# Kernel optimization log

Hardware: AMD Instinct MI355X
Metric: run time of the kernel (lower is better)

Reference implementation:

```python
import jax, jax.numpy as jnp
jax.config.update("jax_enable_x64", True)  # original computes in float64
import numpy as np

ALPHA = 0.01  # init kwarg


def setup_inputs() -> dict:
    key = jax.random.key(0)
    x = jax.random.normal(key, (8, 8192, 512), dtype=jnp.float32)
    return {"x": x}


def reference(x):
    # x: [B, T, C]
    _, t, _ = x.shape
    # powers = flip(arange(t)) = [t-1, t-2, ..., 0]
    powers = jnp.arange(t - 1, -1, -1, dtype=jnp.float64)
    base = jnp.power(1.0 - ALPHA, powers)          # (1-alpha)^(t-1-i), [T]
    divisor = base.reshape(1, t, 1)                # [1, T, 1]
    weights = base.at[1:].multiply(ALPHA).reshape(1, t, 1)
    out = jnp.cumsum(x.astype(jnp.float64) * weights, axis=1) / divisor
    return out.astype(x.dtype)
```

## Files before the change

kernel.cpp:

```cpp
#include <hip/hip_runtime.h>
#include <math.h>


namespace {
constexpr int B = 8;
constexpr int T = 8192;
constexpr int C = 512;
constexpr float ALPHA = 0.01f;
constexpr float DECAY = 1.0f - ALPHA;
constexpr int CHUNK = 32;
constexpr int K = T / CHUNK;
constexpr int STRIDE4 = C / 4;
constexpr int TPB = C / 4;
constexpr int CTILE = 16;
}

__global__ __launch_bounds__(TPB) void ema_ends_kernel(const float* __restrict__ x,
                                                       float* __restrict__ ends) {
    const int k = blockIdx.x;
    const int b = blockIdx.y;
    const int tid = threadIdx.x;
    const float4* xp = reinterpret_cast<const float4*>(x) +
                       (size_t)(b * T + k * CHUNK) * STRIDE4 + tid;
    float4 y;
    if (k == 0) {
        y = xp[0];
    } else {
        y = make_float4(0.f, 0.f, 0.f, 0.f);
    }
#pragma unroll 8
    for (int t = 0; t < CHUNK; ++t) {
        float4 v = xp[(size_t)t * STRIDE4];
        y.x = DECAY * y.x + ALPHA * v.x;
        y.y = DECAY * y.y + ALPHA * v.y;
        y.z = DECAY * y.z + ALPHA * v.z;
        y.w = DECAY * y.w + ALPHA * v.w;
    }
    reinterpret_cast<float4*>(ends)[(size_t)(b * K + k) * STRIDE4 + tid] = y;
}

__global__ __launch_bounds__(TPB) void ema_carry_kernel(float* __restrict__ ends,
                                                        float decay_chunk) {
    const int b = blockIdx.x;
    const int tid = threadIdx.x;
    float4* ep = reinterpret_cast<float4*>(ends) + (size_t)b * K * STRIDE4 + tid;
    float4 y = make_float4(0.f, 0.f, 0.f, 0.f);
    static_assert(K % CTILE == 0, "");
    for (int base = 0; base < K; base += CTILE) {
        float4 e[CTILE];
#pragma unroll
        for (int i = 0; i < CTILE; ++i)
            e[i] = ep[(size_t)(base + i) * STRIDE4];
#pragma unroll
        for (int i = 0; i < CTILE; ++i) {
            y.x = decay_chunk * y.x + e[i].x;
            y.y = decay_chunk * y.y + e[i].y;
            y.z = decay_chunk * y.z + e[i].z;
            y.w = decay_chunk * y.w + e[i].w;
            ep[(size_t)(base + i) * STRIDE4] = y;
        }
    }
}

__global__ __launch_bounds__(TPB) void ema_scan_kernel(const float* __restrict__ x,
                                                       const float* __restrict__ ends,
                                                       float* __restrict__ out) {
    const int k = blockIdx.x;
    const int b = blockIdx.y;
    const int tid = threadIdx.x;
    const size_t base4 = (size_t)(b * T + k * CHUNK) * STRIDE4 + tid;
    const float4* xp = reinterpret_cast<const float4*>(x) + base4;
    float4* op = reinterpret_cast<float4*>(out) + base4;

    float4 y;
    if (k == 0) {
        y = xp[0];
    } else {
        y = reinterpret_cast<const float4*>(ends)[(size_t)(b * K + (k - 1)) * STRIDE4 + tid];
    }
#pragma unroll 8
    for (int t = 0; t < CHUNK; ++t) {
        float4 v = xp[(size_t)t * STRIDE4];
        y.x = DECAY * y.x + ALPHA * v.x;
        y.y = DECAY * y.y + ALPHA * v.y;
        y.z = DECAY * y.z + ALPHA * v.z;
        y.w = DECAY * y.w + ALPHA * v.w;
        op[(size_t)t * STRIDE4] = y;
    }
}

__global__ __launch_bounds__(TPB) void ema_seq_kernel(const float* __restrict__ x,
                                                      float* __restrict__ out) {
    const int b = blockIdx.x;
    const int tid = threadIdx.x;
    const float4* xp = reinterpret_cast<const float4*>(x) + (size_t)b * T * STRIDE4 + tid;
    float4* op = reinterpret_cast<float4*>(out) + (size_t)b * T * STRIDE4 + tid;
    float4 y = xp[0];
    for (int t = 0; t < T; ++t) {
        float4 v = xp[(size_t)t * STRIDE4];
        y.x = DECAY * y.x + ALPHA * v.x;
        y.y = DECAY * y.y + ALPHA * v.y;
        y.z = DECAY * y.z + ALPHA * v.z;
        y.w = DECAY * y.w + ALPHA * v.w;
        op[(size_t)t * STRIDE4] = y;
    }
}

extern "C" void kernel_launch(void* const* d_in, const int* in_sizes, int n_in,
                              void* d_out, int out_size, void* d_ws, size_t ws_size,
                              hipStream_t stream) {
    (void)in_sizes; (void)n_in; (void)out_size;
    const float* x = reinterpret_cast<const float*>(d_in[0]);
    float* out = reinterpret_cast<float*>(d_out);

    const size_t ws_need = (size_t)B * K * C * sizeof(float);
    const float decay_chunk = (float)pow((double)DECAY, (double)CHUNK);

    if (ws_size >= ws_need) {
        float* ends = reinterpret_cast<float*>(d_ws);
        ema_ends_kernel<<<dim3(K, B), dim3(TPB), 0, stream>>>(x, ends);
        ema_carry_kernel<<<dim3(B), dim3(TPB), 0, stream>>>(ends, decay_chunk);
        ema_scan_kernel<<<dim3(K, B), dim3(TPB), 0, stream>>>(x, ends, out);
    } else {
        ema_seq_kernel<<<dim3(B), dim3(TPB), 0, stream>>>(x, out);
    }
}
```

Baseline: 268.9 us.

## Fuse EMA scan into single-pass decoupled look-back kernel

```diff
diff --git a/kernel.cpp b/kernel.cpp
--- a/kernel.cpp
+++ b/kernel.cpp
@@ -12,51 +12,144 @@
 constexpr int K = T / CHUNK;
 constexpr int STRIDE4 = C / 4;
 constexpr int TPB = C / 4;
-constexpr int CTILE = 16;
+constexpr int NCHUNK = B * K;
+
+constexpr size_t WS_TICKET = 0;
+constexpr size_t WS_STATUS = 256;
+constexpr size_t WS_AGGS   = 16384;
+constexpr size_t WS_INCS   = WS_AGGS + (size_t)NCHUNK * C * sizeof(float);
+constexpr size_t WS_NEED   = WS_INCS + (size_t)NCHUNK * C * sizeof(float);
+constexpr size_t WS_ZERO_BYTES = 16384;
+}
+
+__global__ __launch_bounds__(TPB) void ema_fused_kernel(
+    const float* __restrict__ x, float* __restrict__ out,
+    unsigned int* __restrict__ ticket, unsigned int* __restrict__ status,
+    float4* __restrict__ aggs, float4* __restrict__ incs, float decay_chunk) {
+    const int tid = threadIdx.x;
+    __shared__ unsigned int s_vid;
+    if (tid == 0)
+        s_vid = __hip_atomic_fetch_add(ticket, 1u, __ATOMIC_RELAXED,
+                                       __HIP_MEMORY_SCOPE_AGENT);
+    __syncthreads();
+    const unsigned int vid = s_vid;
+    const int b = vid & (B - 1);
+    const int k = vid >> 3;
+    const int idx = b * K + k;
+
+    const size_t base4 = (size_t)(b * T + k * CHUNK) * STRIDE4 + tid;
+    const float4* xp = reinterpret_cast<const float4*>(x) + base4;
+    float4* op = reinterpret_cast<float4*>(out) + base4;
+
+    float4 y[CHUNK];
+#pragma unroll
+    for (int t = 0; t < CHUNK; ++t) y[t] = xp[(size_t)t * STRIDE4];
+    float4 run;
+    if (k == 0) run = y[0];
+    else        run = make_float4(0.f, 0.f, 0.f, 0.f);
+#pragma unroll
+    for (int t = 0; t < CHUNK; ++t) {
+        run.x = DECAY * run.x + ALPHA * y[t].x;
+        run.y = DECAY * run.y + ALPHA * y[t].y;
+        run.z = DECAY * run.z + ALPHA * y[t].z;
+        run.w = DECAY * run.w + ALPHA * y[t].w;
+        y[t] = run;
+    }
+
+    float4 carry = make_float4(0.f, 0.f, 0.f, 0.f);
+    if (k == 0) {
+        incs[(size_t)idx * STRIDE4 + tid] = run;
+        __syncthreads();
+        if (tid == 0) {
+            __builtin_amdgcn_fence(__ATOMIC_RELEASE, "agent");
+            __hip_atomic_store(&status[idx], 2u, __ATOMIC_RELAXED,
+                               __HIP_MEMORY_SCOPE_AGENT);
+        }
+    } else {
+        aggs[(size_t)idx * STRIDE4 + tid] = run;
+        __syncthreads();
+        if (tid == 0) {
+            __builtin_amdgcn_fence(__ATOMIC_RELEASE, "agent");
+            __hip_atomic_store(&status[idx], 1u, __ATOMIC_RELAXED,
+                               __HIP_MEMORY_SCOPE_AGENT);
+        }
+        float w = 1.f;
+        int m = idx - 1;
+        for (;;) {
+            unsigned int s;
+            do {
+                s = __hip_atomic_load(&status[m], __ATOMIC_RELAXED,
+                                      __HIP_MEMORY_SCOPE_AGENT);
+                if (s == 0u) __builtin_amdgcn_s_sleep(1);
+            } while (s == 0u);
+            __builtin_amdgcn_fence(__ATOMIC_ACQUIRE, "agent");
+            if (s == 2u) {
+                float4 v = incs[(size_t)m * STRIDE4 + tid];
+                carry.x += w * v.x; carry.y += w * v.y;
+                carry.z += w * v.z; carry.w += w * v.w;
+                break;
+            } else {
+                float4 v = aggs[(size_t)m * STRIDE4 + tid];
+                carry.x += w * v.x; carry.y += w * v.y;
+                carry.z += w * v.z; carry.w += w * v.w;
+                w *= decay_chunk;
+                --m;
+            }
+        }
+        float4 inc;
+        inc.x = decay_chunk * carry.x + run.x;
+        inc.y = decay_chunk * carry.y + run.y;
+        inc.z = decay_chunk * carry.z + run.z;
+        inc.w = decay_chunk * carry.w + run.w;
+        incs[(size_t)idx * STRIDE4 + tid] = inc;
+        __syncthreads();
+        if (tid == 0) {
+            __builtin_amdgcn_fence(__ATOMIC_RELEASE, "agent");
+            __hip_atomic_store(&status[idx], 2u, __ATOMIC_RELAXED,
+                               __HIP_MEMORY_SCOPE_AGENT);
+        }
+    }
+
+    float w = DECAY;
+#pragma unroll
+    for (int t = 0; t < CHUNK; ++t) {
+        float4 o = y[t];
+        o.x += w * carry.x; o.y += w * carry.y;
+        o.z += w * carry.z; o.w += w * carry.w;
+        op[(size_t)t * STRIDE4] = o;
+        w *= DECAY;
+    }
 }
 
 __global__ __launch_bounds__(TPB) void ema_ends_kernel(const float* __restrict__ x,
                                                        float* __restrict__ ends) {
-    const int k = blockIdx.x;
-    const int b = blockIdx.y;
-    const int tid = threadIdx.x;
+    const int k = blockIdx.x, b = blockIdx.y, tid = threadIdx.x;
     const float4* xp = reinterpret_cast<const float4*>(x) +
                        (size_t)(b * T + k * CHUNK) * STRIDE4 + tid;
-    float4 y;
-    if (k == 0) {
-        y = xp[0];
-    } else {
-        y = make_float4(0.f, 0.f, 0.f, 0.f);
-    }
+    float4 y = (k == 0) ? xp[0] : make_float4(0.f, 0.f, 0.f, 0.f);
 #pragma unroll 8
     for (int t = 0; t < CHUNK; ++t) {
         float4 v = xp[(size_t)t * STRIDE4];
-        y.x = DECAY * y.x + ALPHA * v.x;
-        y.y = DECAY * y.y + ALPHA * v.y;
-        y.z = DECAY * y.z + ALPHA * v.z;
-        y.w = DECAY * y.w + ALPHA * v.w;
+        y.x = DECAY * y.x + ALPHA * v.x; y.y = DECAY * y.y + ALPHA * v.y;
+        y.z = DECAY * y.z + ALPHA * v.z; y.w = DECAY * y.w + ALPHA * v.w;
     }
     reinterpret_cast<float4*>(ends)[(size_t)(b * K + k) * STRIDE4 + tid] = y;
 }
 
 __global__ __launch_bounds__(TPB) void ema_carry_kernel(float* __restrict__ ends,
                                                         float decay_chunk) {
-    const int b = blockIdx.x;
-    const int tid = threadIdx.x;
+    constexpr int CTILE = 16;
+    const int b = blockIdx.x, tid = threadIdx.x;
     float4* ep = reinterpret_cast<float4*>(ends) + (size_t)b * K * STRIDE4 + tid;
     float4 y = make_float4(0.f, 0.f, 0.f, 0.f);
-    static_assert(K % CTILE == 0, "");
     for (int base = 0; base < K; base += CTILE) {
         float4 e[CTILE];
 #pragma unroll
-        for (int i = 0; i < CTILE; ++i)
-            e[i] = ep[(size_t)(base + i) * STRIDE4];
+        for (int i = 0; i < CTILE; ++i) e[i] = ep[(size_t)(base + i) * STRIDE4];
 #pragma unroll
         for (int i = 0; i < CTILE; ++i) {
-            y.x = decay_chunk * y.x + e[i].x;
-            y.y = decay_chunk * y.y + e[i].y;
-            y.z = decay_chunk * y.z + e[i].z;
-            y.w = decay_chunk * y.w + e[i].w;
+            y.x = decay_chunk * y.x + e[i].x; y.y = decay_chunk * y.y + e[i].y;
+            y.z = decay_chunk * y.z + e[i].z; y.w = decay_chunk * y.w + e[i].w;
             ep[(size_t)(base + i) * STRIDE4] = y;
         }
     }
@@ -65,43 +158,17 @@
 __global__ __launch_bounds__(TPB) void ema_scan_kernel(const float* __restrict__ x,
                                                        const float* __restrict__ ends,
                                                        float* __restrict__ out) {
-    const int k = blockIdx.x;
-    const int b = blockIdx.y;
-    const int tid = threadIdx.x;
+    const int k = blockIdx.x, b = blockIdx.y, tid = threadIdx.x;
     const size_t base4 = (size_t)(b * T + k * CHUNK) * STRIDE4 + tid;
     const float4* xp = reinterpret_cast<const float4*>(x) + base4;
     float4* op = reinterpret_cast<float4*>(out) + base4;
-
-    float4 y;
-    if (k == 0) {
-        y = xp[0];
-    } else {
-        y = reinterpret_cast<const float4*>(ends)[(size_t)(b * K + (k - 1)) * STRIDE4 + tid];
-    }
+    float4 y = (k == 0) ? xp[0]
+        : reinterpret_cast<const float4*>(ends)[(size_t)(b * K + (k - 1)) * STRIDE4 + tid];
 #pragma unroll 8
     for (int t = 0; t < CHUNK; ++t) {
         float4 v = xp[(size_t)t * STRIDE4];
-        y.x = DECAY * y.x + ALPHA * v.x;
-        y.y = DECAY * y.y + ALPHA * v.y;
-        y.z = DECAY * y.z + ALPHA * v.z;
-        y.w = DECAY * y.w + ALPHA * v.w;
-        op[(size_t)t * STRIDE4] = y;
-    }
-}
-
-__global__ __launch_bounds__(TPB) void ema_seq_kernel(const float* __restrict__ x,
-                                                      float* __restrict__ out) {
-    const int b = blockIdx.x;
-    const int tid = threadIdx.x;
-    const float4* xp = reinterpret_cast<const float4*>(x) + (size_t)b * T * STRIDE4 + tid;
-    float4* op = reinterpret_cast<float4*>(out) + (size_t)b * T * STRIDE4 + tid;
-    float4 y = xp[0];
-    for (int t = 0; t < T; ++t) {
-        float4 v = xp[(size_t)t * STRIDE4];
-        y.x = DECAY * y.x + ALPHA * v.x;
-        y.y = DECAY * y.y + ALPHA * v.y;
-        y.z = DECAY * y.z + ALPHA * v.z;
-        y.w = DECAY * y.w + ALPHA * v.w;
+        y.x = DECAY * y.x + ALPHA * v.x; y.y = DECAY * y.y + ALPHA * v.y;
+        y.z = DECAY * y.z + ALPHA * v.z; y.w = DECAY * y.w + ALPHA * v.w;
         op[(size_t)t * STRIDE4] = y;
     }
 }
@@ -112,16 +179,21 @@
     (void)in_sizes; (void)n_in; (void)out_size;
     const float* x = reinterpret_cast<const float*>(d_in[0]);
     float* out = reinterpret_cast<float*>(d_out);
-
-    const size_t ws_need = (size_t)B * K * C * sizeof(float);
     const float decay_chunk = (float)pow((double)DECAY, (double)CHUNK);
 
-    if (ws_size >= ws_need) {
+    if (ws_size >= WS_NEED) {
+        char* ws = reinterpret_cast<char*>(d_ws);
+        unsigned int* ticket = reinterpret_cast<unsigned int*>(ws + WS_TICKET);
+        unsigned int* status = reinterpret_cast<unsigned int*>(ws + WS_STATUS);
+        float4* aggs = reinterpret_cast<float4*>(ws + WS_AGGS);
+        float4* incs = reinterpret_cast<float4*>(ws + WS_INCS);
+        hipMemsetAsync(d_ws, 0, WS_ZERO_BYTES, stream);
+        ema_fused_kernel<<<dim3(NCHUNK), dim3(TPB), 0, stream>>>(
+            x, out, ticket, status, aggs, incs, decay_chunk);
+    } else if (ws_size >= (size_t)B * K * C * sizeof(float)) {
         float* ends = reinterpret_cast<float*>(d_ws);
         ema_ends_kernel<<<dim3(K, B), dim3(TPB), 0, stream>>>(x, ends);
         ema_carry_kernel<<<dim3(B), dim3(TPB), 0, stream>>>(ends, decay_chunk);
         ema_scan_kernel<<<dim3(K, B), dim3(TPB), 0, stream>>>(x, ends, out);
-    } else {
-        ema_seq_kernel<<<dim3(B), dim3(TPB), 0, stream>>>(x, out);
     }
 }
```

Result: slower. 772.5 us (+187.3%).
